# Kernel tuning notes

Measured on AMD Instinct MI355X. Metric: run time of the kernel, lower is better.

The kernel has to match this reference:

```python
import jax, jax.numpy as jnp
import numpy as np

B, T, C = 4, 2048, 1024

def setup_inputs() -> dict:
    key = jax.random.key(0)
    kx, kq, kk, kv = jax.random.split(key, 4)
    s = C ** -0.5  # match nn.Linear init scale roughly
    return {
        "x": jax.random.normal(kx, (B, T, C), dtype=jnp.float32),
        "Wq": jax.random.normal(kq, (C, C), dtype=jnp.float32) * s,
        "Wk": jax.random.normal(kk, (C, C), dtype=jnp.float32) * s,
        "Wv": jax.random.normal(kv, (C, C), dtype=jnp.float32) * s,
    }

def reference(x, Wq, Wk, Wv):
    Bq, Tq, Cq = x.shape
    # nn.Linear: y = x @ W^T (bias=False)
    q = jnp.einsum('btc,dc->btd', x, Wq)
    k = jnp.einsum('btc,dc->btd', x, Wk)
    v = jnp.einsum('btc,dc->btd', x, Wv)
    scale = Cq ** -0.5
    qk = jnp.einsum('btd,bsd->bts', q, k) * scale  # [B, T, T]
    causal = jnp.tril(jnp.ones((Tq, Tq), dtype=bool))
    qk = jnp.where(causal, qk, -jnp.inf)
    attn = jax.nn.softmax(qk, axis=-1)
    out = jnp.einsum('bts,bsd->btd', attn, v)
    return out
```

## Files before the change

### kernel.cpp

```cpp
#include <hip/hip_runtime.h>
#include <hip/hip_fp16.h>


typedef __attribute__((ext_vector_type(8))) _Float16 half8;
typedef __attribute__((ext_vector_type(4))) _Float16 half4;
typedef __attribute__((ext_vector_type(4))) float f32x4;

#define AS1 __attribute__((address_space(1)))
#define AS3 __attribute__((address_space(3)))

__device__ __forceinline__ void gload_lds16(const void* g, void* l) {
    __builtin_amdgcn_global_load_lds((AS1 void*)g, (AS3 void*)l, 16, 0, 0);
}

template<int TM, int TN, bool SWAP>
__device__ __forceinline__ void gemm_nt_core(
    const _Float16* __restrict__ A, const _Float16* __restrict__ B,
    int lda, int ldb, int k0, int k1,
    _Float16* ldsA, _Float16* ldsB,
    f32x4 acc[TM / 32][TN / 32])
{
    constexpr int FM = TM / 32, FN = TN / 32;
    constexpr int NA = TM / 32, NB = TN / 32;
    const int t    = threadIdx.x;
    const int lane = t & 63;
    const int wm   = (t >> 7) & 1;
    const int wn   = (t >> 6) & 1;
    const int lr   = lane & 15;
    const int lq   = lane >> 4;

    const _Float16* ga[NA]; int loA[NA];
    const _Float16* gb[NB]; int loB[NB];
#pragma unroll
    for (int i = 0; i < NA; ++i) {
        int f = t + 256 * i;
        int r = f >> 3, c = (f & 7) ^ ((f >> 3) & 7);
        ga[i] = A + (size_t)r * lda + c * 8;
        loA[i] = f * 8;
    }
#pragma unroll
    for (int i = 0; i < NB; ++i) {
        int f = t + 256 * i;
        int r = f >> 3, c = (f & 7) ^ ((f >> 3) & 7);
        gb[i] = B + (size_t)r * ldb + c * 8;
        loB[i] = f * 8;
    }

    int offA[2][FM], offB[2][FN];
#pragma unroll
    for (int h = 0; h < 2; ++h) {
#pragma unroll
        for (int i = 0; i < FM; ++i) {
            int R = wm * (TM / 2) + i * 16 + lr;
            offA[h][i] = (8 * R + ((h * 4 + lq) ^ (R & 7))) * 8;
        }
#pragma unroll
        for (int i = 0; i < FN; ++i) {
            int R = wn * (TN / 2) + i * 16 + lr;
            offB[h][i] = (8 * R + ((h * 4 + lq) ^ (R & 7))) * 8;
        }
    }

    for (int k = k0; k < k1; k += 64) {
        __syncthreads();
#pragma unroll
        for (int i = 0; i < NA; ++i) gload_lds16(ga[i] + k, ldsA + loA[i]);
#pragma unroll
        for (int i = 0; i < NB; ++i) gload_lds16(gb[i] + k, ldsB + loB[i]);
        __syncthreads();

#pragma unroll
        for (int h = 0; h < 2; ++h) {
            half8 af[FM], bf[FN];
#pragma unroll
            for (int i = 0; i < FM; ++i) af[i] = *(const half8*)(ldsA + offA[h][i]);
#pragma unroll
            for (int i = 0; i < FN; ++i) bf[i] = *(const half8*)(ldsB + offB[h][i]);
#pragma unroll
            for (int mi = 0; mi < FM; ++mi)
#pragma unroll
                for (int ni = 0; ni < FN; ++ni) {
                    if constexpr (SWAP)
                        acc[mi][ni] = __builtin_amdgcn_mfma_f32_16x16x32_f16(
                            bf[ni], af[mi], acc[mi][ni], 0, 0, 0);
                    else
                        acc[mi][ni] = __builtin_amdgcn_mfma_f32_16x16x32_f16(
                            af[mi], bf[ni], acc[mi][ni], 0, 0, 0);
                }
        }
    }
}

__global__ __launch_bounds__(256) void f32tof16_k(
    const float* __restrict__ in, _Float16* __restrict__ out, int n)
{
    int i = (blockIdx.x * 256 + threadIdx.x) * 4;
    if (i < n) {
        float4 f = *(const float4*)(in + i);
        half4 h = { (_Float16)f.x, (_Float16)f.y, (_Float16)f.z, (_Float16)f.w };
        *(half4*)(out + i) = h;
    }
}

__global__ __launch_bounds__(256) void wconv_k(
    const float* __restrict__ Wq, const float* __restrict__ Wk,
    const float* __restrict__ Wv, _Float16* __restrict__ out)
{
    const float* src = (blockIdx.y == 0) ? Wq : (blockIdx.y == 1) ? Wk : Wv;
    int i = (blockIdx.x * 256 + threadIdx.x) * 4;
    float4 f = *(const float4*)(src + i);
    half4 h = { (_Float16)f.x, (_Float16)f.y, (_Float16)f.z, (_Float16)f.w };
    *(half4*)(out + (size_t)blockIdx.y * 1024 * 1024 + i) = h;
}

__global__ __launch_bounds__(256) void qkv_gemm_k(
    const _Float16* __restrict__ xh, const _Float16* __restrict__ Wh,
    _Float16* __restrict__ Q, _Float16* __restrict__ K, _Float16* __restrict__ Vt)
{
    __shared__ __align__(16) _Float16 ldsA[128 * 64];
    __shared__ __align__(16) _Float16 ldsB[128 * 64];
    const int tileM = blockIdx.x * 128;
    const int tileN = blockIdx.y * 128;
    const int z     = blockIdx.z;
    const _Float16* W = Wh + (size_t)z * 1024 * 1024;

    const int lane = threadIdx.x & 63;
    const int wm = (threadIdx.x >> 7) & 1, wn = (threadIdx.x >> 6) & 1;
    const int lr = lane & 15, lq = lane >> 4;

    if (z == 2) {
        f32x4 acc[4][4] = {};
        gemm_nt_core<128, 128, false>(xh + (size_t)tileM * 1024,
                                      W + (size_t)tileN * 1024,
                                      1024, 1024, 0, 1024, ldsA, ldsB, acc);
#pragma unroll
        for (int mi = 0; mi < 4; ++mi)
#pragma unroll
            for (int ni = 0; ni < 4; ++ni) {
                int m0 = tileM + wm * 64 + mi * 16 + lq * 4;
                int n  = tileN + wn * 64 + ni * 16 + lr;
                int b = m0 >> 11, tt = m0 & 2047;
                half4 h = { (_Float16)acc[mi][ni][0], (_Float16)acc[mi][ni][1],
                            (_Float16)acc[mi][ni][2], (_Float16)acc[mi][ni][3] };
                *(half4*)(Vt + (size_t)b * 2048 * 1024 + (size_t)n * 2048 + tt) = h;
            }
    } else {
        f32x4 acc[4][4] = {};
        gemm_nt_core<128, 128, true>(xh + (size_t)tileM * 1024,
                                     W + (size_t)tileN * 1024,
                                     1024, 1024, 0, 1024, ldsA, ldsB, acc);
        _Float16* O = (z == 0) ? Q : K;
#pragma unroll
        for (int mi = 0; mi < 4; ++mi)
#pragma unroll
            for (int ni = 0; ni < 4; ++ni) {
                int tt = tileM + wm * 64 + mi * 16 + lr;
                int d0 = tileN + wn * 64 + ni * 16 + lq * 4;
                half4 h = { (_Float16)acc[mi][ni][0], (_Float16)acc[mi][ni][1],
                            (_Float16)acc[mi][ni][2], (_Float16)acc[mi][ni][3] };
                *(half4*)(O + (size_t)tt * 1024 + d0) = h;
            }
    }
}

__global__ __launch_bounds__(256) void scores_gemm_k(
    const _Float16* __restrict__ Q, const _Float16* __restrict__ K,
    _Float16* __restrict__ S)
{
    const int ti = blockIdx.x, si = blockIdx.y;
    if (si > ti) return;
    const int tileT = ti * 128, tileS = si * 128, b = blockIdx.z;

    __shared__ __align__(16) _Float16 ldsA[128 * 64];
    __shared__ __align__(16) _Float16 ldsB[128 * 64];
    f32x4 acc[4][4] = {};
    gemm_nt_core<128, 128, true>(
        Q + (size_t)b * 2048 * 1024 + (size_t)tileT * 1024,
        K + (size_t)b * 2048 * 1024 + (size_t)tileS * 1024,
        1024, 1024, 0, 1024, ldsA, ldsB, acc);

    const int lane = threadIdx.x & 63;
    const int wm = (threadIdx.x >> 7) & 1, wn = (threadIdx.x >> 6) & 1;
    const int lr = lane & 15, lq = lane >> 4;
    const float scale = 0.03125f;

#pragma unroll
    for (int mi = 0; mi < 4; ++mi)
#pragma unroll
        for (int ni = 0; ni < 4; ++ni) {
            int tt = tileT + wm * 64 + mi * 16 + lr;
            int s0 = tileS + wn * 64 + ni * 16 + lq * 4;
            half4 h;
#pragma unroll
            for (int r = 0; r < 4; ++r)
                h[r] = (s0 + r <= tt) ? (_Float16)(acc[mi][ni][r] * scale)
                                      : (_Float16)0.f;
            *(half4*)(S + ((size_t)b * 2048 + tt) * 2048 + s0) = h;
        }
}

__global__ __launch_bounds__(256) void softmax_k(_Float16* __restrict__ S)
{
    const int w    = threadIdx.x >> 6;
    const int lane = threadIdx.x & 63;
    const int t    = blockIdx.x * 4 + w;
    const int b    = blockIdx.y;
    _Float16* row = S + ((size_t)b * 2048 + t) * 2048;

    float x[32];
    float mx = -1e30f;
#pragma unroll
    for (int j = 0; j < 4; ++j) {
        half8 h = *(const half8*)(row + j * 512 + lane * 8);
#pragma unroll
        for (int e = 0; e < 8; ++e) {
            int s = j * 512 + lane * 8 + e;
            float f = (s <= t) ? (float)h[e] : -1e30f;
            x[j * 8 + e] = f;
            mx = fmaxf(mx, f);
        }
    }
#pragma unroll
    for (int o = 32; o > 0; o >>= 1) mx = fmaxf(mx, __shfl_xor(mx, o));

    float sum = 0.f;
#pragma unroll
    for (int i = 0; i < 32; ++i) {
        float e = __expf(x[i] - mx);
        x[i] = e;
        sum += e;
    }
#pragma unroll
    for (int o = 32; o > 0; o >>= 1) sum += __shfl_xor(sum, o);
    const float inv = 1.0f / sum;

#pragma unroll
    for (int j = 0; j < 4; ++j) {
        half8 p;
#pragma unroll
        for (int e = 0; e < 8; ++e) p[e] = (_Float16)(x[j * 8 + e] * inv);
        *(half8*)(row + j * 512 + lane * 8) = p;
    }
}

__global__ __launch_bounds__(256) void pv_gemm_k(
    const _Float16* __restrict__ P, const _Float16* __restrict__ Vt,
    float* __restrict__ out)
{
    __shared__ __align__(16) _Float16 ldsA[128 * 64];
    __shared__ __align__(16) _Float16 ldsB[64 * 64];
    const int tileT = (15 - blockIdx.x) * 128;
    const int tileD = blockIdx.y * 64;
    const int b     = blockIdx.z;
    const int kEnd  = tileT + 128;

    f32x4 acc[4][2] = {};
    gemm_nt_core<128, 64, true>(
        P + ((size_t)b * 2048 + tileT) * 2048,
        Vt + (size_t)b * 1024 * 2048 + (size_t)tileD * 2048,
        2048, 2048, 0, kEnd, ldsA, ldsB, acc);

    const int lane = threadIdx.x & 63;
    const int wm = (threadIdx.x >> 7) & 1, wn = (threadIdx.x >> 6) & 1;
    const int lr = lane & 15, lq = lane >> 4;

#pragma unroll
    for (int mi = 0; mi < 4; ++mi)
#pragma unroll
        for (int ni = 0; ni < 2; ++ni) {
            int tt = tileT + wm * 64 + mi * 16 + lr;
            int d0 = tileD + wn * 32 + ni * 16 + lq * 4;
            *(f32x4*)(out + ((size_t)b * 2048 + tt) * 1024 + d0) = acc[mi][ni];
        }
}

extern "C" void kernel_launch(void* const* d_in, const int* in_sizes, int n_in,
                              void* d_out, int out_size, void* d_ws, size_t ws_size,
                              hipStream_t stream)
{
    const float* x  = (const float*)d_in[0];
    const float* Wq = (const float*)d_in[1];
    const float* Wk = (const float*)d_in[2];
    const float* Wv = (const float*)d_in[3];
    float* out = (float*)d_out;

    char* ws = (char*)d_ws;
    _Float16* xh = (_Float16*)(ws);
    _Float16* Wh = (_Float16*)(ws + (16u << 20));
    _Float16* Qh = (_Float16*)(ws + (22u << 20));
    _Float16* Kh = (_Float16*)(ws + (38u << 20));
    _Float16* Vt = (_Float16*)(ws + (54u << 20));
    _Float16* S  = (_Float16*)(ws + (70u << 20));

    f32tof16_k<<<8192, 256, 0, stream>>>(x, xh, 4 * 2048 * 1024);
    wconv_k<<<dim3(1024, 3), 256, 0, stream>>>(Wq, Wk, Wv, Wh);

    qkv_gemm_k<<<dim3(64, 8, 3), 256, 0, stream>>>(xh, Wh, Qh, Kh, Vt);

    scores_gemm_k<<<dim3(16, 16, 4), 256, 0, stream>>>(Qh, Kh, S);
    softmax_k<<<dim3(512, 4), 256, 0, stream>>>(S);
    pv_gemm_k<<<dim3(16, 16, 4), 256, 0, stream>>>(S, Vt, out);
}
```

Measured before the change: 262.8 us.

## Enlarge GEMM tiles and generalize warp layout in gemm core

Generalizes the shared GEMM core to a configurable warp grid. The QKV and score GEMMs now use 256x128 tiles with four warps stacked along M, and the PV GEMM uses 128x128 tiles instead of 128x64. Larger tiles raise arithmetic intensity and cut redundant global/LDS loads. The cost is more accumulator registers and LDS per block, which lowers occupancy. Fewer blocks may also leave some CUs idle or unbalanced, especially on the causal score grid where the coarser tiles do some wasted masked work.

```diff
diff --git a/kernel.cpp b/kernel.cpp
--- a/kernel.cpp
+++ b/kernel.cpp
@@ -13,19 +13,20 @@
     __builtin_amdgcn_global_load_lds((AS1 void*)g, (AS3 void*)l, 16, 0, 0);
 }
 
-template<int TM, int TN, bool SWAP>
+template<int TM, int TN, int WM, int WN, bool SWAP>
 __device__ __forceinline__ void gemm_nt_core(
     const _Float16* __restrict__ A, const _Float16* __restrict__ B,
     int lda, int ldb, int k0, int k1,
     _Float16* ldsA, _Float16* ldsB,
-    f32x4 acc[TM / 32][TN / 32])
-{
-    constexpr int FM = TM / 32, FN = TN / 32;
+    f32x4 acc[TM / (WM * 16)][TN / (WN * 16)])
+{
+    constexpr int FM = TM / (WM * 16), FN = TN / (WN * 16);
     constexpr int NA = TM / 32, NB = TN / 32;
     const int t    = threadIdx.x;
     const int lane = t & 63;
-    const int wm   = (t >> 7) & 1;
-    const int wn   = (t >> 6) & 1;
+    const int w    = t >> 6;
+    const int wm   = w % WM;
+    const int wn   = w / WM;
     const int lr   = lane & 15;
     const int lq   = lane >> 4;
 
@@ -51,12 +52,12 @@
     for (int h = 0; h < 2; ++h) {
 #pragma unroll
         for (int i = 0; i < FM; ++i) {
-            int R = wm * (TM / 2) + i * 16 + lr;
+            int R = wm * (TM / WM) + i * 16 + lr;
             offA[h][i] = (8 * R + ((h * 4 + lq) ^ (R & 7))) * 8;
         }
 #pragma unroll
         for (int i = 0; i < FN; ++i) {
-            int R = wn * (TN / 2) + i * 16 + lr;
+            int R = wn * (TN / WN) + i * 16 + lr;
             offB[h][i] = (8 * R + ((h * 4 + lq) ^ (R & 7))) * 8;
         }
     }
@@ -117,45 +118,45 @@
     const _Float16* __restrict__ xh, const _Float16* __restrict__ Wh,
     _Float16* __restrict__ Q, _Float16* __restrict__ K, _Float16* __restrict__ Vt)
 {
-    __shared__ __align__(16) _Float16 ldsA[128 * 64];
+    __shared__ __align__(16) _Float16 ldsA[256 * 64];
     __shared__ __align__(16) _Float16 ldsB[128 * 64];
-    const int tileM = blockIdx.x * 128;
+    const int tileM = blockIdx.x * 256;
     const int tileN = blockIdx.y * 128;
     const int z     = blockIdx.z;
     const _Float16* W = Wh + (size_t)z * 1024 * 1024;
 
     const int lane = threadIdx.x & 63;
-    const int wm = (threadIdx.x >> 7) & 1, wn = (threadIdx.x >> 6) & 1;
+    const int wm   = threadIdx.x >> 6;
     const int lr = lane & 15, lq = lane >> 4;
 
     if (z == 2) {
-        f32x4 acc[4][4] = {};
-        gemm_nt_core<128, 128, false>(xh + (size_t)tileM * 1024,
-                                      W + (size_t)tileN * 1024,
-                                      1024, 1024, 0, 1024, ldsA, ldsB, acc);
+        f32x4 acc[4][8] = {};
+        gemm_nt_core<256, 128, 4, 1, false>(xh + (size_t)tileM * 1024,
+                                            W + (size_t)tileN * 1024,
+                                            1024, 1024, 0, 1024, ldsA, ldsB, acc);
 #pragma unroll
         for (int mi = 0; mi < 4; ++mi)
 #pragma unroll
-            for (int ni = 0; ni < 4; ++ni) {
+            for (int ni = 0; ni < 8; ++ni) {
                 int m0 = tileM + wm * 64 + mi * 16 + lq * 4;
-                int n  = tileN + wn * 64 + ni * 16 + lr;
+                int n  = tileN + ni * 16 + lr;
                 int b = m0 >> 11, tt = m0 & 2047;
                 half4 h = { (_Float16)acc[mi][ni][0], (_Float16)acc[mi][ni][1],
                             (_Float16)acc[mi][ni][2], (_Float16)acc[mi][ni][3] };
                 *(half4*)(Vt + (size_t)b * 2048 * 1024 + (size_t)n * 2048 + tt) = h;
             }
     } else {
-        f32x4 acc[4][4] = {};
-        gemm_nt_core<128, 128, true>(xh + (size_t)tileM * 1024,
-                                     W + (size_t)tileN * 1024,
-                                     1024, 1024, 0, 1024, ldsA, ldsB, acc);
+        f32x4 acc[4][8] = {};
+        gemm_nt_core<256, 128, 4, 1, true>(xh + (size_t)tileM * 1024,
+                                           W + (size_t)tileN * 1024,
+                                           1024, 1024, 0, 1024, ldsA, ldsB, acc);
         _Float16* O = (z == 0) ? Q : K;
 #pragma unroll
         for (int mi = 0; mi < 4; ++mi)
 #pragma unroll
-            for (int ni = 0; ni < 4; ++ni) {
+            for (int ni = 0; ni < 8; ++ni) {
                 int tt = tileM + wm * 64 + mi * 16 + lr;
-                int d0 = tileN + wn * 64 + ni * 16 + lq * 4;
+                int d0 = tileN + ni * 16 + lq * 4;
                 half4 h = { (_Float16)acc[mi][ni][0], (_Float16)acc[mi][ni][1],
                             (_Float16)acc[mi][ni][2], (_Float16)acc[mi][ni][3] };
                 *(half4*)(O + (size_t)tt * 1024 + d0) = h;
@@ -168,28 +169,28 @@
     _Float16* __restrict__ S)
 {
     const int ti = blockIdx.x, si = blockIdx.y;
-    if (si > ti) return;
-    const int tileT = ti * 128, tileS = si * 128, b = blockIdx.z;
-
-    __shared__ __align__(16) _Float16 ldsA[128 * 64];
+    if (si > 2 * ti + 1) return;
+    const int tileT = ti * 256, tileS = si * 128, b = blockIdx.z;
+
+    __shared__ __align__(16) _Float16 ldsA[256 * 64];
     __shared__ __align__(16) _Float16 ldsB[128 * 64];
-    f32x4 acc[4][4] = {};
-    gemm_nt_core<128, 128, true>(
+    f32x4 acc[4][8] = {};
+    gemm_nt_core<256, 128, 4, 1, true>(
         Q + (size_t)b * 2048 * 1024 + (size_t)tileT * 1024,
         K + (size_t)b * 2048 * 1024 + (size_t)tileS * 1024,
         1024, 1024, 0, 1024, ldsA, ldsB, acc);
 
     const int lane = threadIdx.x & 63;
-    const int wm = (threadIdx.x >> 7) & 1, wn = (threadIdx.x >> 6) & 1;
+    const int wm   = threadIdx.x >> 6;
     const int lr = lane & 15, lq = lane >> 4;
     const float scale = 0.03125f;
 
 #pragma unroll
     for (int mi = 0; mi < 4; ++mi)
 #pragma unroll
-        for (int ni = 0; ni < 4; ++ni) {
+        for (int ni = 0; ni < 8; ++ni) {
             int tt = tileT + wm * 64 + mi * 16 + lr;
-            int s0 = tileS + wn * 64 + ni * 16 + lq * 4;
+            int s0 = tileS + ni * 16 + lq * 4;
             half4 h;
 #pragma unroll
             for (int r = 0; r < 4; ++r)
@@ -248,28 +249,29 @@
     float* __restrict__ out)
 {
     __shared__ __align__(16) _Float16 ldsA[128 * 64];
-    __shared__ __align__(16) _Float16 ldsB[64 * 64];
+    __shared__ __align__(16) _Float16 ldsB[128 * 64];
     const int tileT = (15 - blockIdx.x) * 128;
-    const int tileD = blockIdx.y * 64;
+    const int tileD = blockIdx.y * 128;
     const int b     = blockIdx.z;
     const int kEnd  = tileT + 128;
 
-    f32x4 acc[4][2] = {};
-    gemm_nt_core<128, 64, true>(
+    f32x4 acc[4][4] = {};
+    gemm_nt_core<128, 128, 2, 2, true>(
         P + ((size_t)b * 2048 + tileT) * 2048,
         Vt + (size_t)b * 1024 * 2048 + (size_t)tileD * 2048,
         2048, 2048, 0, kEnd, ldsA, ldsB, acc);
 
     const int lane = threadIdx.x & 63;
-    const int wm = (threadIdx.x >> 7) & 1, wn = (threadIdx.x >> 6) & 1;
+    const int w    = threadIdx.x >> 6;
+    const int wm = w % 2, wn = w / 2;
     const int lr = lane & 15, lq = lane >> 4;
 
 #pragma unroll
     for (int mi = 0; mi < 4; ++mi)
 #pragma unroll
-        for (int ni = 0; ni < 2; ++ni) {
+        for (int ni = 0; ni < 4; ++ni) {
             int tt = tileT + wm * 64 + mi * 16 + lr;
-            int d0 = tileD + wn * 32 + ni * 16 + lq * 4;
+            int d0 = tileD + wn * 64 + ni * 16 + lq * 4;
             *(f32x4*)(out + ((size_t)b * 2048 + tt) * 1024 + d0) = acc[mi][ni];
         }
 }
@@ -295,9 +297,9 @@
     f32tof16_k<<<8192, 256, 0, stream>>>(x, xh, 4 * 2048 * 1024);
     wconv_k<<<dim3(1024, 3), 256, 0, stream>>>(Wq, Wk, Wv, Wh);
 
-    qkv_gemm_k<<<dim3(64, 8, 3), 256, 0, stream>>>(xh, Wh, Qh, Kh, Vt);
-
-    scores_gemm_k<<<dim3(16, 16, 4), 256, 0, stream>>>(Qh, Kh, S);
+    qkv_gemm_k<<<dim3(32, 8, 3), 256, 0, stream>>>(xh, Wh, Qh, Kh, Vt);
+
+    scores_gemm_k<<<dim3(8, 16, 4), 256, 0, stream>>>(Qh, Kh, S);
     softmax_k<<<dim3(512, 4), 256, 0, stream>>>(S);
-    pv_gemm_k<<<dim3(16, 16, 4), 256, 0, stream>>>(S, Vt, out);
-}
+    pv_gemm_k<<<dim3(16, 8, 4), 256, 0, stream>>>(S, Vt, out);
+}
```

Result: slower. 305.8 us (+16.4%).

## Prefetch next K-tile into registers instead of direct global-to-LDS loads

Applied to the files above, without the earlier changes.

Replaces the direct global-to-LDS loads in the shared GEMM core with register staging. The next 64-wide K slice is loaded into registers while the current slice is consumed by MFMAs, then written to LDS at the top of the next iteration. The aim is to hide global memory latency that was previously exposed between the two barriers of each step. The warp-to-tile mapping is also generalized via template parameters and the wm/wn assignment is swapped, with the epilogues updated to match. The cost is extra VGPRs for the staging registers and explicit LDS store instructions.

```diff
diff --git a/kernel.cpp b/kernel.cpp
--- a/kernel.cpp
+++ b/kernel.cpp
@@ -6,26 +6,20 @@
 typedef __attribute__((ext_vector_type(4))) _Float16 half4;
 typedef __attribute__((ext_vector_type(4))) float f32x4;
 
-#define AS1 __attribute__((address_space(1)))
-#define AS3 __attribute__((address_space(3)))
-
-__device__ __forceinline__ void gload_lds16(const void* g, void* l) {
-    __builtin_amdgcn_global_load_lds((AS1 void*)g, (AS3 void*)l, 16, 0, 0);
-}
-
-template<int TM, int TN, bool SWAP>
+template<int TM, int TN, int WM, int WN, bool SWAP>
 __device__ __forceinline__ void gemm_nt_core(
     const _Float16* __restrict__ A, const _Float16* __restrict__ B,
     int lda, int ldb, int k0, int k1,
     _Float16* ldsA, _Float16* ldsB,
-    f32x4 acc[TM / 32][TN / 32])
-{
-    constexpr int FM = TM / 32, FN = TN / 32;
+    f32x4 acc[TM / (WM * 16)][TN / (WN * 16)])
+{
+    constexpr int FM = TM / (WM * 16), FN = TN / (WN * 16);
     constexpr int NA = TM / 32, NB = TN / 32;
     const int t    = threadIdx.x;
     const int lane = t & 63;
-    const int wm   = (t >> 7) & 1;
-    const int wn   = (t >> 6) & 1;
+    const int w    = t >> 6;
+    const int wm   = w % WM;
+    const int wn   = w / WM;
     const int lr   = lane & 15;
     const int lq   = lane >> 4;
 
@@ -51,22 +45,34 @@
     for (int h = 0; h < 2; ++h) {
 #pragma unroll
         for (int i = 0; i < FM; ++i) {
-            int R = wm * (TM / 2) + i * 16 + lr;
+            int R = wm * (TM / WM) + i * 16 + lr;
             offA[h][i] = (8 * R + ((h * 4 + lq) ^ (R & 7))) * 8;
         }
 #pragma unroll
         for (int i = 0; i < FN; ++i) {
-            int R = wn * (TN / 2) + i * 16 + lr;
+            int R = wn * (TN / WN) + i * 16 + lr;
             offB[h][i] = (8 * R + ((h * 4 + lq) ^ (R & 7))) * 8;
         }
     }
+
+    half8 va[NA], vb[NB];
+#pragma unroll
+    for (int i = 0; i < NA; ++i) va[i] = *(const half8*)(ga[i] + k0);
+#pragma unroll
+    for (int i = 0; i < NB; ++i) vb[i] = *(const half8*)(gb[i] + k0);
 
     for (int k = k0; k < k1; k += 64) {
         __syncthreads();
 #pragma unroll
-        for (int i = 0; i < NA; ++i) gload_lds16(ga[i] + k, ldsA + loA[i]);
-#pragma unroll
-        for (int i = 0; i < NB; ++i) gload_lds16(gb[i] + k, ldsB + loB[i]);
+        for (int i = 0; i < NA; ++i) *(half8*)(ldsA + loA[i]) = va[i];
+#pragma unroll
+        for (int i = 0; i < NB; ++i) *(half8*)(ldsB + loB[i]) = vb[i];
+        if (k + 64 < k1) {
+#pragma unroll
+            for (int i = 0; i < NA; ++i) va[i] = *(const half8*)(ga[i] + k + 64);
+#pragma unroll
+            for (int i = 0; i < NB; ++i) vb[i] = *(const half8*)(gb[i] + k + 64);
+        }
         __syncthreads();
 
 #pragma unroll
@@ -125,14 +131,15 @@
     const _Float16* W = Wh + (size_t)z * 1024 * 1024;
 
     const int lane = threadIdx.x & 63;
-    const int wm = (threadIdx.x >> 7) & 1, wn = (threadIdx.x >> 6) & 1;
+    const int w    = threadIdx.x >> 6;
+    const int wm = w & 1, wn = w >> 1;
     const int lr = lane & 15, lq = lane >> 4;
 
     if (z == 2) {
         f32x4 acc[4][4] = {};
-        gemm_nt_core<128, 128, false>(xh + (size_t)tileM * 1024,
-                                      W + (size_t)tileN * 1024,
-                                      1024, 1024, 0, 1024, ldsA, ldsB, acc);
+        gemm_nt_core<128, 128, 2, 2, false>(xh + (size_t)tileM * 1024,
+                                            W + (size_t)tileN * 1024,
+                                            1024, 1024, 0, 1024, ldsA, ldsB, acc);
 #pragma unroll
         for (int mi = 0; mi < 4; ++mi)
 #pragma unroll
@@ -146,9 +153,9 @@
             }
     } else {
         f32x4 acc[4][4] = {};
-        gemm_nt_core<128, 128, true>(xh + (size_t)tileM * 1024,
-                                     W + (size_t)tileN * 1024,
-                                     1024, 1024, 0, 1024, ldsA, ldsB, acc);
+        gemm_nt_core<128, 128, 2, 2, true>(xh + (size_t)tileM * 1024,
+                                           W + (size_t)tileN * 1024,
+                                           1024, 1024, 0, 1024, ldsA, ldsB, acc);
         _Float16* O = (z == 0) ? Q : K;
 #pragma unroll
         for (int mi = 0; mi < 4; ++mi)
@@ -174,13 +181,14 @@
     __shared__ __align__(16) _Float16 ldsA[128 * 64];
     __shared__ __align__(16) _Float16 ldsB[128 * 64];
     f32x4 acc[4][4] = {};
-    gemm_nt_core<128, 128, true>(
+    gemm_nt_core<128, 128, 2, 2, true>(
         Q + (size_t)b * 2048 * 1024 + (size_t)tileT * 1024,
         K + (size_t)b * 2048 * 1024 + (size_t)tileS * 1024,
         1024, 1024, 0, 1024, ldsA, ldsB, acc);
 
     const int lane = threadIdx.x & 63;
-    const int wm = (threadIdx.x >> 7) & 1, wn = (threadIdx.x >> 6) & 1;
+    const int w    = threadIdx.x >> 6;
+    const int wm = w & 1, wn = w >> 1;
     const int lr = lane & 15, lq = lane >> 4;
     const float scale = 0.03125f;
 
@@ -255,13 +263,14 @@
     const int kEnd  = tileT + 128;
 
     f32x4 acc[4][2] = {};
-    gemm_nt_core<128, 64, true>(
+    gemm_nt_core<128, 64, 2, 2, true>(
         P + ((size_t)b * 2048 + tileT) * 2048,
         Vt + (size_t)b * 1024 * 2048 + (size_t)tileD * 2048,
         2048, 2048, 0, kEnd, ldsA, ldsB, acc);
 
     const int lane = threadIdx.x & 63;
-    const int wm = (threadIdx.x >> 7) & 1, wn = (threadIdx.x >> 6) & 1;
+    const int w    = threadIdx.x >> 6;
+    const int wm = w & 1, wn = w >> 1;
     const int lr = lane & 15, lq = lane >> 4;
 
 #pragma unroll
```

Result: no change. 261.9 us (-0.3%).
